# Optimization experiments

Hardware: AMD Instinct MI355X
Metric: run time of the kernel (lower is better)

## Reference

```python
import jax, jax.numpy as jnp
import numpy as np

BLOCK = 32  # GGUF Q8_0 block size
O, I = 4096, 4096
NB = I // BLOCK  # blocks per output row
B, S = 2, 2048


def setup_inputs() -> dict:
    key = jax.random.key(0)
    k1, k2, k3, k4 = jax.random.split(key, 4)
    x = jax.random.normal(k1, (B, S, I), dtype=jnp.float32)
    # signed int8 quants stored as int32 (values in [-128, 127])
    q_weight = jax.random.randint(k2, (O, I), 0, 256, dtype=jnp.int32) - 128
    # per-block fp scales (small positive, as produced by Q8_0 quantization)
    scales = jax.random.uniform(k3, (O, NB), dtype=jnp.float32) * 0.02 + 1e-4
    bias = jax.random.normal(k4, (O,), dtype=jnp.float32)
    return {"x": x, "q_weight": q_weight, "scales": scales, "bias": bias}


def dequantize(q_weight, scales, dtype):
    # q_weight: [O, I] int, scales: [O, NB] float; block-wise dequant (Q8_0)
    q = q_weight.reshape(O, NB, BLOCK).astype(dtype)
    w = q * scales.astype(dtype)[:, :, None]
    return w.reshape(O, I)  # [O, I]


def reference(x, q_weight, scales, bias):
    # cast_bias_weight: dequantize weight/bias to the input dtype, then linear
    dtype = x.dtype
    w = dequantize(q_weight, scales, dtype)          # [O, I]
    y = jnp.einsum('bsi,oi->bso', x, w) + bias.astype(dtype)
    return y
```

## Files before the change

### kernel.cpp

```cpp
#include <hip/hip_runtime.h>
#include <hip/hip_bf16.h>
#include <stdint.h>


#define M_DIM 4096
#define N_DIM 4096
#define K_DIM 4096
#define NB_SC 128

#define BM 256
#define BN 256
#define BKB 128
#define NT (K_DIM / BKB)
#define TILE_B (BM * BKB)

typedef __attribute__((ext_vector_type(4))) int i32x4;

__device__ __forceinline__ void gload_lds16(const void* gsrc, void* ldsdst) {
  __builtin_amdgcn_global_load_lds(
      (__attribute__((address_space(1))) void*)(uintptr_t)gsrc,
      (__attribute__((address_space(3))) void*)(uint32_t)(uintptr_t)ldsdst,
      16, 0, 0);
}

__device__ __forceinline__ int pack4(int a, int b, int c, int d) {
  return (a & 255) | ((b & 255) << 8) | ((c & 255) << 16) | ((d & 255) << 24);
}


__global__ void prep_kernel(const float* __restrict__ x, const int* __restrict__ q,
                            const float* __restrict__ sc,
                            char* __restrict__ xb, char* __restrict__ wb,
                            float* __restrict__ sxv, float* __restrict__ swv) {
  __shared__ float red[4];
  const int b = blockIdx.x;
  const int t = threadIdx.x;
  if (b < 4096) {
    const float4* row = (const float4*)(x + (size_t)b * K_DIM);
    float4 v[4];
    float m = 0.f;
#pragma unroll
    for (int i = 0; i < 4; ++i) {
      v[i] = row[t * 4 + i];
      m = fmaxf(m, fmaxf(fmaxf(fabsf(v[i].x), fabsf(v[i].y)),
                         fmaxf(fabsf(v[i].z), fabsf(v[i].w))));
    }
#pragma unroll
    for (int off = 32; off >= 1; off >>= 1) m = fmaxf(m, __shfl_xor(m, off, 64));
    if ((t & 63) == 0) red[t >> 6] = m;
    __syncthreads();
    m = fmaxf(fmaxf(red[0], red[1]), fmaxf(red[2], red[3]));
    const float inv = (m > 0.f) ? 127.0f / m : 0.f;
    int4 o;
    o.x = pack4(__float2int_rn(v[0].x * inv), __float2int_rn(v[0].y * inv),
                __float2int_rn(v[0].z * inv), __float2int_rn(v[0].w * inv));
    o.y = pack4(__float2int_rn(v[1].x * inv), __float2int_rn(v[1].y * inv),
                __float2int_rn(v[1].z * inv), __float2int_rn(v[1].w * inv));
    o.z = pack4(__float2int_rn(v[2].x * inv), __float2int_rn(v[2].y * inv),
                __float2int_rn(v[2].z * inv), __float2int_rn(v[2].w * inv));
    o.w = pack4(__float2int_rn(v[3].x * inv), __float2int_rn(v[3].y * inv),
                __float2int_rn(v[3].z * inv), __float2int_rn(v[3].w * inv));
    ((int4*)(xb + (size_t)b * K_DIM))[t] = o;
    if (t == 0) sxv[b] = m / 127.0f;
  } else {
    const int o_row = b - 4096;
    float m = sc[o_row * NB_SC + (t & 127)];
#pragma unroll
    for (int off = 32; off >= 1; off >>= 1) m = fmaxf(m, __shfl_xor(m, off, 64));
    if ((t & 63) == 0) red[t >> 6] = m;
    __syncthreads();
    m = fmaxf(fmaxf(red[0], red[1]), fmaxf(red[2], red[3]));
    const float ratio = sc[o_row * NB_SC + (t >> 1)] / m;
    const int4* qp = (const int4*)(q + (size_t)o_row * K_DIM);
    int4 qv[4];
#pragma unroll
    for (int i = 0; i < 4; ++i) qv[i] = qp[t * 4 + i];
    int4 ov;
    ov.x = pack4(__float2int_rn((float)qv[0].x * ratio), __float2int_rn((float)qv[0].y * ratio),
                 __float2int_rn((float)qv[0].z * ratio), __float2int_rn((float)qv[0].w * ratio));
    ov.y = pack4(__float2int_rn((float)qv[1].x * ratio), __float2int_rn((float)qv[1].y * ratio),
                 __float2int_rn((float)qv[1].z * ratio), __float2int_rn((float)qv[1].w * ratio));
    ov.z = pack4(__float2int_rn((float)qv[2].x * ratio), __float2int_rn((float)qv[2].y * ratio),
                 __float2int_rn((float)qv[2].z * ratio), __float2int_rn((float)qv[2].w * ratio));
    ov.w = pack4(__float2int_rn((float)qv[3].x * ratio), __float2int_rn((float)qv[3].y * ratio),
                 __float2int_rn((float)qv[3].z * ratio), __float2int_rn((float)qv[3].w * ratio));
    ((int4*)(wb + (size_t)o_row * K_DIM))[t] = ov;
    if (t == 0) swv[o_row] = m;
  }
}


__device__ __forceinline__ void stage_half(const char* __restrict__ pX,
                                           char* lds, int hr0, int ktb, int w) {
#pragma unroll
  for (int j = 0; j < 2; ++j) {
    gload_lds16(pX + (size_t)(hr0 + j * 8) * K_DIM + ktb,
                lds + (hr0 + w * 16 + j * 8) * BKB);
  }
}

template <int BUF, int Q>
__device__ __forceinline__ void read_aq(const char* pa0, const char* pa1,
                                        i32x4 (&af)[2][2]) {
#pragma unroll
  for (int j = 0; j < 2; ++j) {
    af[j][0] = *(const i32x4*)(pa0 + BUF * TILE_B + (Q * 32 + j * 16) * BKB);
    af[j][1] = *(const i32x4*)(pa1 + BUF * TILE_B + (Q * 32 + j * 16) * BKB);
  }
}

template <int BUF>
__device__ __forceinline__ void read_ball(const char* pb0, const char* pb1,
                                          i32x4 (&bf)[4][2]) {
#pragma unroll
  for (int ni = 0; ni < 4; ++ni) {
    bf[ni][0] = *(const i32x4*)(pb0 + BUF * TILE_B + ni * 16 * BKB);
    bf[ni][1] = *(const i32x4*)(pb1 + BUF * TILE_B + ni * 16 * BKB);
  }
}

__device__ __forceinline__ void mfma_quad(const i32x4 (&af)[2][2], const i32x4 (&bf)[4][2],
                                          i32x4 (&acc)[8][4], int q0) {
  __builtin_amdgcn_s_setprio(1);
#pragma unroll
  for (int q = 0; q < 2; ++q)
#pragma unroll
    for (int ni = 0; ni < 4; ++ni)
#pragma unroll
      for (int kk = 0; kk < 2; ++kk)
        acc[q0 + q][ni] =
            __builtin_amdgcn_mfma_i32_16x16x64_i8(af[q][kk], bf[ni][kk], acc[q0 + q][ni], 0, 0, 0);
  __builtin_amdgcn_s_setprio(0);
}

template <int AB, int BB, int MODE>
__device__ __forceinline__ void ktile(const char* pa0, const char* pa1,
                                      const char* pb0, const char* pb1,
                                      const char* __restrict__ pA,
                                      const char* __restrict__ pB,
                                      char* AsB, char* BsB,
                                      int ktb, int w,
                                      i32x4 (&acc)[8][4]) {
  char* An = AsB + (AB ^ 1) * TILE_B;
  char* Bw = BsB + ((BB + 2) % 3) * TILE_B;

  if (MODE < 2) {
    stage_half(pA, An, 0, ktb + BKB, w);
    stage_half(pA, An, 128, ktb + BKB, w);
  }
  if (MODE == 0) {
    stage_half(pB, Bw, 0, ktb + 2 * BKB, w);
    stage_half(pB, Bw, 128, ktb + 2 * BKB, w);
  }

  i32x4 bf[4][2];
  i32x4 a0[2][2], a1[2][2], a2[2][2], a3[2][2];
  read_ball<BB>(pb0, pb1, bf);
  read_aq<AB, 0>(pa0, pa1, a0);
  mfma_quad(a0, bf, acc, 0);
  read_aq<AB, 1>(pa0, pa1, a1);
  mfma_quad(a1, bf, acc, 2);
  read_aq<AB, 2>(pa0, pa1, a2);
  mfma_quad(a2, bf, acc, 4);
  read_aq<AB, 3>(pa0, pa1, a3);
  mfma_quad(a3, bf, acc, 6);

  if (MODE < 2) {
    asm volatile("s_waitcnt lgkmcnt(0)" ::: "memory");
    if (MODE == 0)
      asm volatile("s_waitcnt vmcnt(4)" ::: "memory");
    else
      asm volatile("s_waitcnt vmcnt(0)" ::: "memory");
    __builtin_amdgcn_s_barrier();
    __builtin_amdgcn_sched_barrier(0);
  }
}

__global__ __launch_bounds__(512, 2) void gemm256(const char* __restrict__ A,
                                                  const char* __restrict__ B,
                                                  const float* __restrict__ sxv,
                                                  const float* __restrict__ swv,
                                                  const float* __restrict__ bias,
                                                  float* __restrict__ C) {
  __shared__ char AsB[2 * TILE_B];
  __shared__ char BsB[3 * TILE_B];

  const int tid = threadIdx.x;
  const int w = tid >> 6;
  const int l = tid & 63;
  const int wm = w >> 2;
  const int wn = w & 3;
  const int frow = l & 15;
  const int fkb = (l >> 4) * 16;

  const int bid = blockIdx.x;
  const int cpx = gridDim.x >> 3;
  const int swz = (bid & 7) * cpx + (bid >> 3);
  const int bm0 = (swz >> 4) * BM;
  const int bn0 = (swz & 15) * BN;

  const int fr7 = frow & 7;
  const int sw0 = (((fkb) >> 4) ^ fr7) << 4;
  const int sw1 = (((fkb + 64) >> 4) ^ fr7) << 4;
  const char* pa0 = (const char*)AsB + (wm * 128 + frow) * BKB + sw0;
  const char* pa1 = (const char*)AsB + (wm * 128 + frow) * BKB + sw1;
  const char* pb0 = (const char*)BsB + (wn * 64 + frow) * BKB + sw0;
  const char* pb1 = (const char*)BsB + (wn * 64 + frow) * BKB + sw1;

  const int sr = l >> 3;
  const int skp = ((l & 7) ^ sr) << 4;
  const char* pA = A + (size_t)(bm0 + w * 16 + sr) * K_DIM + skp;
  const char* pB = B + (size_t)(bn0 + w * 16 + sr) * K_DIM + skp;

  i32x4 acc[8][4] = {};

  stage_half(pA, AsB, 0, 0, w);
  stage_half(pA, AsB, 128, 0, w);
  stage_half(pB, BsB, 0, 0, w);
  stage_half(pB, BsB, 128, 0, w);
  stage_half(pB, BsB + TILE_B, 0, BKB, w);
  stage_half(pB, BsB + TILE_B, 128, BKB, w);
  asm volatile("s_waitcnt vmcnt(4)" ::: "memory");
  __builtin_amdgcn_s_barrier();

  for (int t = 0; t < NT - 2; t += 6) {
    ktile<0, 0, 0>(pa0, pa1, pb0, pb1, pA, pB, AsB, BsB, (t + 0) * BKB, w, acc);
    ktile<1, 1, 0>(pa0, pa1, pb0, pb1, pA, pB, AsB, BsB, (t + 1) * BKB, w, acc);
    ktile<0, 2, 0>(pa0, pa1, pb0, pb1, pA, pB, AsB, BsB, (t + 2) * BKB, w, acc);
    ktile<1, 0, 0>(pa0, pa1, pb0, pb1, pA, pB, AsB, BsB, (t + 3) * BKB, w, acc);
    ktile<0, 1, 0>(pa0, pa1, pb0, pb1, pA, pB, AsB, BsB, (t + 4) * BKB, w, acc);
    ktile<1, 2, 0>(pa0, pa1, pb0, pb1, pA, pB, AsB, BsB, (t + 5) * BKB, w, acc);
  }
  ktile<0, 0, 1>(pa0, pa1, pb0, pb1, pA, pB, AsB, BsB, (NT - 2) * BKB, w, acc);
  ktile<1, 1, 2>(pa0, pa1, pb0, pb1, pA, pB, AsB, BsB, (NT - 1) * BKB, w, acc);

#pragma unroll
  for (int ni = 0; ni < 4; ++ni) {
    const int n = bn0 + wn * 64 + ni * 16 + (l & 15);
    const float swn = swv[n];
    const float bv = bias[n];
#pragma unroll
    for (int mi = 0; mi < 8; ++mi) {
      const int mbase = bm0 + wm * 128 + mi * 16 + (l >> 4) * 4;
#pragma unroll
      for (int r = 0; r < 4; ++r)
        C[(size_t)(mbase + r) * N_DIM + n] =
            (float)acc[mi][ni][r] * (swn * sxv[mbase + r]) + bv;
    }
  }
}


__global__ void naive_kernel(const float* __restrict__ x, const int* __restrict__ q,
                             const float* __restrict__ sc, const float* __restrict__ bias,
                             float* __restrict__ out) {
  size_t idx = (size_t)blockIdx.x * blockDim.x + threadIdx.x;
  if (idx >= (size_t)M_DIM * N_DIM) return;
  int n = (int)(idx & (N_DIM - 1));
  size_t m = idx >> 12;
  float acc = 0.f;
  for (int k = 0; k < K_DIM; k += 32) {
    float s = sc[n * NB_SC + (k >> 5)];
    float part = 0.f;
    for (int j = 0; j < 32; ++j)
      part += x[m * K_DIM + k + j] * (float)q[(size_t)n * K_DIM + k + j];
    acc += part * s;
  }
  out[idx] = acc + bias[n];
}


extern "C" void kernel_launch(void* const* d_in, const int* in_sizes, int n_in,
                              void* d_out, int out_size, void* d_ws, size_t ws_size,
                              hipStream_t stream) {
  const float* x    = (const float*)d_in[0];
  const int*   q    = (const int*)d_in[1];
  const float* sc   = (const float*)d_in[2];
  const float* bias = (const float*)d_in[3];
  float* out = (float*)d_out;

  const size_t elems = (size_t)M_DIM * K_DIM;
  const size_t need  = 2 * elems + 2 * 4096 * sizeof(float);

  if (ws_size >= need) {
    char* xb = (char*)d_ws;
    char* wb = xb + elems;
    float* sxv = (float*)(wb + elems);
    float* swv = sxv + 4096;
    hipLaunchKernelGGL(prep_kernel, dim3(8192), dim3(256), 0, stream,
                       x, q, sc, xb, wb, sxv, swv);
    hipLaunchKernelGGL(gemm256, dim3((M_DIM / BM) * (N_DIM / BN)), dim3(512), 0, stream,
                       xb, wb, sxv, swv, bias, out);
  } else {
    hipLaunchKernelGGL(naive_kernel, dim3((M_DIM * N_DIM) / 256), dim3(256), 0, stream,
                       x, q, sc, bias, out);
  }
}
```

Baseline: 92.65 us.

## Shrink GEMM tile to 128x256 with 64-byte K steps and new LDS swizzle

```diff
diff --git a/kernel.cpp b/kernel.cpp
--- a/kernel.cpp
+++ b/kernel.cpp
@@ -8,11 +8,12 @@
 #define K_DIM 4096
 #define NB_SC 128
 
-#define BM 256
+#define BM 128
 #define BN 256
-#define BKB 128
+#define BKB 64
 #define NT (K_DIM / BKB)
-#define TILE_B (BM * BKB)
+#define TILE_A (BM * BKB)
+#define TILE_BN (BN * BKB)
 
 typedef __attribute__((ext_vector_type(4))) int i32x4;
 
@@ -90,85 +91,51 @@
 }
 
 
-__device__ __forceinline__ void stage_half(const char* __restrict__ pX,
-                                           char* lds, int hr0, int ktb, int w) {
-#pragma unroll
-  for (int j = 0; j < 2; ++j) {
-    gload_lds16(pX + (size_t)(hr0 + j * 8) * K_DIM + ktb,
-                lds + (hr0 + w * 16 + j * 8) * BKB);
-  }
-}
-
-template <int BUF, int Q>
-__device__ __forceinline__ void read_aq(const char* pa0, const char* pa1,
-                                        i32x4 (&af)[2][2]) {
-#pragma unroll
-  for (int j = 0; j < 2; ++j) {
-    af[j][0] = *(const i32x4*)(pa0 + BUF * TILE_B + (Q * 32 + j * 16) * BKB);
-    af[j][1] = *(const i32x4*)(pa1 + BUF * TILE_B + (Q * 32 + j * 16) * BKB);
-  }
-}
-
-template <int BUF>
-__device__ __forceinline__ void read_ball(const char* pb0, const char* pb1,
-                                          i32x4 (&bf)[4][2]) {
-#pragma unroll
-  for (int ni = 0; ni < 4; ++ni) {
-    bf[ni][0] = *(const i32x4*)(pb0 + BUF * TILE_B + ni * 16 * BKB);
-    bf[ni][1] = *(const i32x4*)(pb1 + BUF * TILE_B + ni * 16 * BKB);
-  }
-}
-
-__device__ __forceinline__ void mfma_quad(const i32x4 (&af)[2][2], const i32x4 (&bf)[4][2],
-                                          i32x4 (&acc)[8][4], int q0) {
+__device__ __forceinline__ void stage_unit(const char* __restrict__ pX,
+                                           char* ldsdst, int w) {
+  gload_lds16(pX, ldsdst + w * 1024);
+}
+
+__device__ __forceinline__ void mfma_all(const i32x4 (&af)[4], const i32x4 (&bf)[4],
+                                         i32x4 (&acc)[4][4]) {
   __builtin_amdgcn_s_setprio(1);
 #pragma unroll
-  for (int q = 0; q < 2; ++q)
-#pragma unroll
-    for (int ni = 0; ni < 4; ++ni)
-#pragma unroll
-      for (int kk = 0; kk < 2; ++kk)
-        acc[q0 + q][ni] =
-            __builtin_amdgcn_mfma_i32_16x16x64_i8(af[q][kk], bf[ni][kk], acc[q0 + q][ni], 0, 0, 0);
+  for (int a = 0; a < 4; ++a)
+#pragma unroll
+    for (int b = 0; b < 4; ++b)
+      acc[a][b] = __builtin_amdgcn_mfma_i32_16x16x64_i8(af[a], bf[b], acc[a][b], 0, 0, 0);
   __builtin_amdgcn_s_setprio(0);
 }
 
 template <int AB, int BB, int MODE>
-__device__ __forceinline__ void ktile(const char* pa0, const char* pa1,
-                                      const char* pb0, const char* pb1,
+__device__ __forceinline__ void ktile(const char* pa, const char* pb,
                                       const char* __restrict__ pA,
                                       const char* __restrict__ pB,
                                       char* AsB, char* BsB,
                                       int ktb, int w,
-                                      i32x4 (&acc)[8][4]) {
-  char* An = AsB + (AB ^ 1) * TILE_B;
-  char* Bw = BsB + ((BB + 2) % 3) * TILE_B;
-
-  if (MODE < 2) {
-    stage_half(pA, An, 0, ktb + BKB, w);
-    stage_half(pA, An, 128, ktb + BKB, w);
-  }
+                                      i32x4 (&acc)[4][4]) {
+  if (MODE < 2)
+    stage_unit(pA + ktb + BKB, AsB + (AB ^ 1) * TILE_A, w);
   if (MODE == 0) {
-    stage_half(pB, Bw, 0, ktb + 2 * BKB, w);
-    stage_half(pB, Bw, 128, ktb + 2 * BKB, w);
-  }
-
-  i32x4 bf[4][2];
-  i32x4 a0[2][2], a1[2][2], a2[2][2], a3[2][2];
-  read_ball<BB>(pb0, pb1, bf);
-  read_aq<AB, 0>(pa0, pa1, a0);
-  mfma_quad(a0, bf, acc, 0);
-  read_aq<AB, 1>(pa0, pa1, a1);
-  mfma_quad(a1, bf, acc, 2);
-  read_aq<AB, 2>(pa0, pa1, a2);
-  mfma_quad(a2, bf, acc, 4);
-  read_aq<AB, 3>(pa0, pa1, a3);
-  mfma_quad(a3, bf, acc, 6);
+#pragma unroll
+    for (int u = 0; u < 2; ++u)
+      stage_unit(pB + (size_t)u * 128 * K_DIM + ktb + 2 * BKB,
+                 BsB + ((BB + 2) % 3) * TILE_BN + u * 8192, w);
+  }
+
+  i32x4 af[4], bf[4];
+#pragma unroll
+  for (int f = 0; f < 4; ++f)
+    bf[f] = *(const i32x4*)(pb + BB * TILE_BN + f * 1024);
+#pragma unroll
+  for (int f = 0; f < 4; ++f)
+    af[f] = *(const i32x4*)(pa + AB * TILE_A + f * 1024);
+  mfma_all(af, bf, acc);
 
   if (MODE < 2) {
     asm volatile("s_waitcnt lgkmcnt(0)" ::: "memory");
     if (MODE == 0)
-      asm volatile("s_waitcnt vmcnt(4)" ::: "memory");
+      asm volatile("s_waitcnt vmcnt(2)" ::: "memory");
     else
       asm volatile("s_waitcnt vmcnt(0)" ::: "memory");
     __builtin_amdgcn_s_barrier();
@@ -176,14 +143,14 @@
   }
 }
 
-__global__ __launch_bounds__(512, 2) void gemm256(const char* __restrict__ A,
+__global__ __launch_bounds__(512, 4) void gemm128(const char* __restrict__ A,
                                                   const char* __restrict__ B,
                                                   const float* __restrict__ sxv,
                                                   const float* __restrict__ swv,
                                                   const float* __restrict__ bias,
                                                   float* __restrict__ C) {
-  __shared__ char AsB[2 * TILE_B];
-  __shared__ char BsB[3 * TILE_B];
+  __shared__ char AsB[2 * TILE_A];
+  __shared__ char BsB[3 * TILE_BN];
 
   const int tid = threadIdx.x;
   const int w = tid >> 6;
@@ -191,7 +158,7 @@
   const int wm = w >> 2;
   const int wn = w & 3;
   const int frow = l & 15;
-  const int fkb = (l >> 4) * 16;
+  const int gl = l >> 4;
 
   const int bid = blockIdx.x;
   const int cpx = gridDim.x >> 3;
@@ -199,53 +166,51 @@
   const int bm0 = (swz >> 4) * BM;
   const int bn0 = (swz & 15) * BN;
 
-  const int fr7 = frow & 7;
-  const int sw0 = (((fkb) >> 4) ^ fr7) << 4;
-  const int sw1 = (((fkb + 64) >> 4) ^ fr7) << 4;
-  const char* pa0 = (const char*)AsB + (wm * 128 + frow) * BKB + sw0;
-  const char* pa1 = (const char*)AsB + (wm * 128 + frow) * BKB + sw1;
-  const char* pb0 = (const char*)BsB + (wn * 64 + frow) * BKB + sw0;
-  const char* pb1 = (const char*)BsB + (wn * 64 + frow) * BKB + sw1;
-
-  const int sr = l >> 3;
-  const int skp = ((l & 7) ^ sr) << 4;
+  const int srow = (frow & 3) ^ ((frow >> 2) & 3);
+  const int swg = ((gl ^ srow) << 4);
+  const char* pa = (const char*)AsB + (wm * 64 + frow) * BKB + swg;
+  const char* pb = (const char*)BsB + (wn * 64 + frow) * BKB + swg;
+
+  const int sr = l >> 2;
+  const int skp = ((((l & 3) ^ ((l >> 2) & 3)) ^ ((l >> 4) & 3)) << 4);
   const char* pA = A + (size_t)(bm0 + w * 16 + sr) * K_DIM + skp;
   const char* pB = B + (size_t)(bn0 + w * 16 + sr) * K_DIM + skp;
 
-  i32x4 acc[8][4] = {};
-
-  stage_half(pA, AsB, 0, 0, w);
-  stage_half(pA, AsB, 128, 0, w);
-  stage_half(pB, BsB, 0, 0, w);
-  stage_half(pB, BsB, 128, 0, w);
-  stage_half(pB, BsB + TILE_B, 0, BKB, w);
-  stage_half(pB, BsB + TILE_B, 128, BKB, w);
-  asm volatile("s_waitcnt vmcnt(4)" ::: "memory");
+  i32x4 acc[4][4] = {};
+
+  stage_unit(pA, AsB, w);
+  stage_unit(pB, BsB, w);
+  stage_unit(pB + (size_t)128 * K_DIM, BsB + 8192, w);
+  stage_unit(pB + BKB, BsB + TILE_BN, w);
+  stage_unit(pB + (size_t)128 * K_DIM + BKB, BsB + TILE_BN + 8192, w);
+  asm volatile("s_waitcnt vmcnt(2)" ::: "memory");
   __builtin_amdgcn_s_barrier();
 
-  for (int t = 0; t < NT - 2; t += 6) {
-    ktile<0, 0, 0>(pa0, pa1, pb0, pb1, pA, pB, AsB, BsB, (t + 0) * BKB, w, acc);
-    ktile<1, 1, 0>(pa0, pa1, pb0, pb1, pA, pB, AsB, BsB, (t + 1) * BKB, w, acc);
-    ktile<0, 2, 0>(pa0, pa1, pb0, pb1, pA, pB, AsB, BsB, (t + 2) * BKB, w, acc);
-    ktile<1, 0, 0>(pa0, pa1, pb0, pb1, pA, pB, AsB, BsB, (t + 3) * BKB, w, acc);
-    ktile<0, 1, 0>(pa0, pa1, pb0, pb1, pA, pB, AsB, BsB, (t + 4) * BKB, w, acc);
-    ktile<1, 2, 0>(pa0, pa1, pb0, pb1, pA, pB, AsB, BsB, (t + 5) * BKB, w, acc);
-  }
-  ktile<0, 0, 1>(pa0, pa1, pb0, pb1, pA, pB, AsB, BsB, (NT - 2) * BKB, w, acc);
-  ktile<1, 1, 2>(pa0, pa1, pb0, pb1, pA, pB, AsB, BsB, (NT - 1) * BKB, w, acc);
-
-#pragma unroll
-  for (int ni = 0; ni < 4; ++ni) {
-    const int n = bn0 + wn * 64 + ni * 16 + (l & 15);
+  for (int t = 0; t < NT - 4; t += 6) {
+    ktile<0, 0, 0>(pa, pb, pA, pB, AsB, BsB, (t + 0) * BKB, w, acc);
+    ktile<1, 1, 0>(pa, pb, pA, pB, AsB, BsB, (t + 1) * BKB, w, acc);
+    ktile<0, 2, 0>(pa, pb, pA, pB, AsB, BsB, (t + 2) * BKB, w, acc);
+    ktile<1, 0, 0>(pa, pb, pA, pB, AsB, BsB, (t + 3) * BKB, w, acc);
+    ktile<0, 1, 0>(pa, pb, pA, pB, AsB, BsB, (t + 4) * BKB, w, acc);
+    ktile<1, 2, 0>(pa, pb, pA, pB, AsB, BsB, (t + 5) * BKB, w, acc);
+  }
+  ktile<0, 0, 0>(pa, pb, pA, pB, AsB, BsB, (NT - 4) * BKB, w, acc);
+  ktile<1, 1, 0>(pa, pb, pA, pB, AsB, BsB, (NT - 3) * BKB, w, acc);
+  ktile<0, 2, 1>(pa, pb, pA, pB, AsB, BsB, (NT - 2) * BKB, w, acc);
+  ktile<1, 0, 2>(pa, pb, pA, pB, AsB, BsB, (NT - 1) * BKB, w, acc);
+
+#pragma unroll
+  for (int nb = 0; nb < 4; ++nb) {
+    const int n = bn0 + wn * 64 + nb * 16 + (l & 15);
     const float swn = swv[n];
     const float bv = bias[n];
 #pragma unroll
-    for (int mi = 0; mi < 8; ++mi) {
-      const int mbase = bm0 + wm * 128 + mi * 16 + (l >> 4) * 4;
+    for (int ma = 0; ma < 4; ++ma) {
+      const int mbase = bm0 + wm * 64 + ma * 16 + (l >> 4) * 4;
 #pragma unroll
       for (int r = 0; r < 4; ++r)
         C[(size_t)(mbase + r) * N_DIM + n] =
-            (float)acc[mi][ni][r] * (swn * sxv[mbase + r]) + bv;
+            (float)acc[ma][nb][r] * (swn * sxv[mbase + r]) + bv;
     }
   }
 }
@@ -289,7 +254,7 @@
     float* swv = sxv + 4096;
     hipLaunchKernelGGL(prep_kernel, dim3(8192), dim3(256), 0, stream,
                        x, q, sc, xb, wb, sxv, swv);
-    hipLaunchKernelGGL(gemm256, dim3((M_DIM / BM) * (N_DIM / BN)), dim3(512), 0, stream,
+    hipLaunchKernelGGL(gemm128, dim3((M_DIM / BM) * (N_DIM / BN)), dim3(512), 0, stream,
                        xb, wb, sxv, swv, bias, out);
   } else {
     hipLaunchKernelGGL(naive_kernel, dim3((M_DIM * N_DIM) / 256), dim3(256), 0, stream,
```

New measurement: 102.5 us. 1.11x slower.
